# Optimization experiments

Hardware: AMD Instinct MI355X
Metric: run time of the kernel (lower is better)

## Reference

```python
import jax, jax.numpy as jnp
import numpy as np

B, S, D, H = 2, 2048, 1024, 16
HD = D // H

def setup_inputs() -> dict:
    key = jax.random.key(0)
    ks = jax.random.split(key, 9)
    s = 1.0 / np.sqrt(D)
    inp = {"x": jax.random.normal(ks[0], (B, S, D), dtype=jnp.float32)}
    for i, name in enumerate(["q", "k", "v", "o"]):
        inp[f"W_{name}"] = jax.random.uniform(ks[1 + 2 * i], (D, D), dtype=jnp.float32, minval=-s, maxval=s)
        inp[f"b_{name}"] = jax.random.uniform(ks[2 + 2 * i], (D,), dtype=jnp.float32, minval=-s, maxval=s)
    return inp


def reference(x, W_q, b_q, W_k, b_k, W_v, b_v, W_o, b_o):
    # x: [B, S, D]
    def split_heads(t):
        return t.reshape(B, S, H, HD).transpose(0, 2, 1, 3)  # [B, H, S, HD]

    Q = split_heads(x @ W_q + b_q)
    K = split_heads(x @ W_k + b_k)
    V = split_heads(x @ W_v + b_v)

    scale = 1.0 / np.sqrt(HD).astype(np.float32)
    scores = jnp.einsum("bhqd,bhkd->bhqk", Q, K) * scale  # [B, H, S, S]
    weights = jax.nn.softmax(scores, axis=-1)
    attn = jnp.einsum("bhqk,bhkd->bhqd", weights, V)  # [B, H, S, HD]
    attn = attn.transpose(0, 2, 1, 3).reshape(B, S, D)
    return attn @ W_o + b_o
```

## Files before the change

### kernel.cpp

```cpp
#include <hip/hip_runtime.h>
#include <hip/hip_bf16.h>

#define BB 2
#define SS 2048
#define DD 1024
#define HH 16
#define HD 64

typedef __attribute__((ext_vector_type(8))) short bf16x8;
typedef __attribute__((ext_vector_type(4))) float f32x4;

__device__ __forceinline__ unsigned short f2bf(float f) {
  unsigned int u = __float_as_uint(f);
  return (unsigned short)((u + 0x7FFFu + ((u >> 16) & 1u)) >> 16);
}

__device__ __forceinline__ float fast_exp2(float x) {
#if __has_builtin(__builtin_amdgcn_exp2f)
  return __builtin_amdgcn_exp2f(x);
#else
  return __expf(x * 0.6931471805599453f);
#endif
}

__device__ __forceinline__ void async_copy16(const unsigned short* gp, unsigned short* lp) {
  __builtin_amdgcn_global_load_lds(
      (const __attribute__((address_space(1))) unsigned int*)gp,
      (__attribute__((address_space(3))) unsigned int*)lp, 16, 0, 0);
}

__device__ __forceinline__ void pl32_swap(unsigned& a, unsigned& b) {
#if __has_builtin(__builtin_amdgcn_permlane32_swap)
  auto r = __builtin_amdgcn_permlane32_swap(a, b, false, false);
  a = r[0];
  b = r[1];
#else
  asm volatile("v_permlane32_swap_b32 %0, %1" : "+v"(a), "+v"(b));
#endif
}
__device__ __forceinline__ void pl16_swap(unsigned& a, unsigned& b) {
#if __has_builtin(__builtin_amdgcn_permlane16_swap)
  auto r = __builtin_amdgcn_permlane16_swap(a, b, false, false);
  a = r[0];
  b = r[1];
#else
  asm volatile("v_permlane16_swap_b32 %0, %1" : "+v"(a), "+v"(b));
#endif
}

__global__ __launch_bounds__(256) void prep_kernel(
    const float* __restrict__ x, unsigned short* __restrict__ xb,
    const float* __restrict__ W0, unsigned short* __restrict__ T0,
    const float* __restrict__ W1, unsigned short* __restrict__ T1,
    const float* __restrict__ W2, unsigned short* __restrict__ T2,
    const float* __restrict__ W3, unsigned short* __restrict__ T3) {
  const int blk = blockIdx.x;
  const int t = threadIdx.x;
  if (blk < 4096) {
    int i = blk * 1024 + t * 4;
    float4 v = *(const float4*)(x + i);
    ushort4 u;
    u.x = f2bf(v.x); u.y = f2bf(v.y); u.z = f2bf(v.z); u.w = f2bf(v.w);
    *(ushort4*)(xb + i) = u;
    return;
  }
  const int j = blk - 4096;
  const int jw = j >> 10;
  const int tb = j & 1023;
  const float* W = jw == 0 ? W0 : (jw == 1 ? W1 : (jw == 2 ? W2 : W3));
  unsigned short* T = jw == 0 ? T0 : (jw == 1 ? T1 : (jw == 2 ? T2 : T3));
  __shared__ float tile[32][33];
  int k0 = (tb & 31) * 32, n0 = (tb >> 5) * 32;
  int c = t & 31, r0 = t >> 5;
#pragma unroll
  for (int i = 0; i < 4; ++i) {
    int r = r0 + i * 8;
    tile[r][c] = W[(size_t)(k0 + r) * DD + n0 + c];
  }
  __syncthreads();
#pragma unroll
  for (int i = 0; i < 4; ++i) {
    int r = r0 + i * 8;
    T[(size_t)(n0 + r) * DD + k0 + c] = f2bf(tile[c][r]);
  }
}

template <int STORE>
__device__ __forceinline__ void gemm_core(
    const unsigned short* __restrict__ A, const unsigned short* __restrict__ BT,
    const float* __restrict__ bias, void* __restrict__ outp, float scale,
    int bm, int bn) {
  const int t = threadIdx.x;
  const int w = t >> 6;
  const int l = t & 63;
  const int wm = (w >> 1) * 64;
  const int wn = (w & 1) * 64;

  __shared__ __align__(16) unsigned short As[128 * 32];
  __shared__ __align__(16) unsigned short Bs[128 * 32];

  f32x4 acc[4][4];
#pragma unroll
  for (int i = 0; i < 4; ++i)
#pragma unroll
    for (int j = 0; j < 4; ++j) acc[i][j] = (f32x4)0.f;

  const int fr = l & 15;
  const int kg = (l >> 4) * 8;

  for (int k0 = 0; k0 < DD; k0 += 32) {
    __syncthreads();
#pragma unroll
    for (int c = 0; c < 2; ++c) {
      int e = (w * 2 + c) * 512 + l * 8;
      int row = e >> 5, kk = e & 31;
      async_copy16(A + (size_t)(bm + row) * DD + k0 + kk, As + (w * 2 + c) * 512);
      async_copy16(BT + (size_t)(bn + row) * DD + k0 + kk, Bs + (w * 2 + c) * 512);
    }
    __syncthreads();

    bf16x8 af[4], bfr[4];
#pragma unroll
    for (int i = 0; i < 4; ++i)
      af[i] = *(const bf16x8*)(As + (wm + i * 16 + fr) * 32 + kg);
#pragma unroll
    for (int j = 0; j < 4; ++j)
      bfr[j] = *(const bf16x8*)(Bs + (wn + j * 16 + fr) * 32 + kg);
#pragma unroll
    for (int i = 0; i < 4; ++i)
#pragma unroll
      for (int j = 0; j < 4; ++j)
        acc[i][j] = __builtin_amdgcn_mfma_f32_16x16x32_bf16(af[i], bfr[j], acc[i][j], 0, 0, 0);
  }

  const int col_l = l & 15;
  const int row_l = (l >> 4) * 4;

#pragma unroll
  for (int i = 0; i < 4; ++i) {
    int m_base = bm + wm + i * 16 + row_l;
#pragma unroll
    for (int j = 0; j < 4; ++j) {
      int n = bn + wn + j * 16 + col_l;
      float bv = bias[n];
      float* out = (float*)outp;
#pragma unroll
      for (int r = 0; r < 4; ++r)
        out[(size_t)(m_base + r) * DD + n] = acc[i][j][r] + bv;
    }
  }
}

__global__ __launch_bounds__(256) void out_gemm_mfma(
    const unsigned short* __restrict__ A, const unsigned short* __restrict__ WoT,
    const float* __restrict__ bo, float* __restrict__ out) {
  const int i = blockIdx.x;
  const int xcd = i & 7;
  const int slot = i >> 3;
  const int bm = (xcd + 8 * (slot >> 3)) * 128;
  const int bn = (slot & 7) * 128;
  gemm_core<0>(A, WoT, bo, (void*)out, 1.0f, bm, bn);
}

#define QPHASE(DB, KH, MH, S, VM) do {                                        \
    bf16x8 af[4];                                                             \
    _Pragma("unroll")                                                         \
    for (int ii = 0; ii < 4; ++ii) {                                          \
      int row = wm * 128 + (MH) * 64 + ii * 16 + fr;                          \
      int kb = kg16 ^ ((row & 8) ? 32 : 0) ^ ((row & 4) ? 16 : 0);            \
      af[ii] = *(const bf16x8*)((const char*)&lds[0][DB][KH][0] + row * 64 + kb); \
    }                                                                         \
    if ((MH) == 0) {                                                          \
      _Pragma("unroll")                                                       \
      for (int j = 0; j < 4; ++j) {                                           \
        int row = wn * 64 + j * 16 + fr;                                      \
        int kb = kg16 ^ ((row & 8) ? 32 : 0) ^ ((row & 4) ? 16 : 0);          \
        bfr[j] = *(const bf16x8*)((const char*)&lds[1][DB][KH][0] + row * 64 + kb); \
      }                                                                       \
    }                                                                         \
    stage_half(S);                                                            \
    asm volatile("s_barrier" ::: "memory");                                   \
    __builtin_amdgcn_s_setprio(1);                                            \
    _Pragma("unroll")                                                         \
    for (int ii = 0; ii < 4; ++ii)                                            \
      _Pragma("unroll")                                                       \
      for (int j = 0; j < 4; ++j)                                             \
        acc[(MH) * 4 + ii][j] = __builtin_amdgcn_mfma_f32_16x16x32_bf16(      \
            af[ii], bfr[j], acc[(MH) * 4 + ii][j], 0, 0, 0);                  \
    __builtin_amdgcn_s_setprio(0);                                            \
    if ((VM) == 1) asm volatile("s_waitcnt vmcnt(4)" ::: "memory");           \
    if ((VM) == 2) asm volatile("s_waitcnt vmcnt(0)" ::: "memory");           \
    asm volatile("s_barrier" ::: "memory");                                   \
  } while (0)

__global__ __launch_bounds__(512, 2) void qkv_gemm_8ph(
    const unsigned short* __restrict__ A,
    const unsigned short* __restrict__ WqT, const unsigned short* __restrict__ WkT,
    const unsigned short* __restrict__ WvT,
    const float* __restrict__ bq, const float* __restrict__ bk,
    const float* __restrict__ bv,
    unsigned short* __restrict__ Qo, unsigned short* __restrict__ Ko,
    unsigned short* __restrict__ VTo) {
  const int i = blockIdx.x;
  const int xcd = i & 7;
  const int slot = i >> 3;
  const int bmi = xcd * 2 + (slot / 12);
  const int c = slot % 12;
  const int which = c >> 2;
  const int bm = bmi * 256;
  const int bn = (c & 3) * 256;
  const unsigned short* BT = which == 0 ? WqT : (which == 1 ? WkT : WvT);
  const float* bias = which == 0 ? bq : (which == 1 ? bk : bv);

  const int t = threadIdx.x;
  const int w = t >> 6;
  const int l = t & 63;
  const int wm = w >> 2;
  const int wn = w & 3;
  const int fr = l & 15;
  const int kg16 = (l >> 4) * 16;

  __shared__ __align__(16) unsigned short lds[2][2][2][8192];

  f32x4 acc[8][4];
#pragma unroll
  for (int mi = 0; mi < 8; ++mi)
#pragma unroll
    for (int j = 0; j < 4; ++j) acc[mi][j] = (f32x4)0.f;

  auto stage_half = [&](int s) {
    if (s >= 64) return;
    const int Ts = s >> 2;
    const int db = Ts & 1;
    const int typ = s & 3;
    const int kh = typ >> 1;
    const int isB = typ & 1;
    const unsigned short* src = isB ? BT : A;
    const int rbase = isB ? bn : bm;
    unsigned short* dstbase = &lds[isB][db][kh][0];
    const int k0 = Ts * 64 + kh * 32;
#pragma unroll
    for (int j = 0; j < 2; ++j) {
      int cc = (w * 2 + j) * 64 + l;
      int row = cc >> 2;
      int ke = ((cc & 3) * 8) ^ ((row & 8) ? 16 : 0) ^ ((row & 4) ? 8 : 0);
      async_copy16(src + (size_t)(rbase + row) * DD + k0 + ke,
                   dstbase + (w * 2 + j) * 512);
    }
  };

  bf16x8 bfr[4];

  for (int s = 0; s < 6; ++s) stage_half(s);
  asm volatile("s_waitcnt vmcnt(4)" ::: "memory");
  asm volatile("s_barrier" ::: "memory");

  for (int T = 0; T < 14; ++T) {
    const int db = T & 1;
    const int sb = 4 * T + 6;
    QPHASE(db, 0, 0, sb + 0, 0);
    QPHASE(db, 0, 1, sb + 1, 0);
    QPHASE(db, 1, 0, sb + 2, 0);
    QPHASE(db, 1, 1, sb + 3, 1);
  }
  QPHASE(0, 0, 0, 62, 0);
  QPHASE(0, 0, 1, 63, 0);
  QPHASE(0, 1, 0, 64, 0);
  QPHASE(0, 1, 1, 64, 2);
  QPHASE(1, 0, 0, 64, 0);
  QPHASE(1, 0, 1, 64, 0);
  QPHASE(1, 1, 0, 64, 0);
  QPHASE(1, 1, 1, 64, 0);

  const int col_l = l & 15;
  const int row_l = (l >> 4) * 4;
  const int b_ = bm >> 11;

  if (which != 2) {
    const float scl = which == 0 ? 0.18033688011112042f : 1.0f;
    unsigned short* out = which == 0 ? Qo : Ko;
#pragma unroll
    for (int mi = 0; mi < 8; ++mi) {
      int m_base = bm + wm * 128 + mi * 16 + row_l;
#pragma unroll
      for (int j = 0; j < 4; ++j) {
        int n = bn + wn * 64 + j * 16 + col_l;
        float bv = bias[n];
        int h_ = n >> 6, hd_ = n & 63;
#pragma unroll
        for (int r = 0; r < 4; ++r) {
          int m = m_base + r;
          int b2 = m >> 11, s_ = m & 2047;
          out[(((size_t)(b2 * HH + h_) * SS) + s_) * HD + hd_] =
              f2bf((acc[mi][j][r] + bv) * scl);
        }
      }
    }
  } else {
    unsigned int* Tt = (unsigned int*)&lds[0][0][0][0];
#pragma unroll
    for (int mi = 0; mi < 8; ++mi) {
      int m2a = wm * 64 + mi * 8 + (l >> 4) * 2;
#pragma unroll
      for (int j = 0; j < 4; ++j) {
        int n = wn * 64 + j * 16 + col_l;
        float bv = bias[bn + n];
        uint2 dd;
        dd.x = (unsigned)f2bf(acc[mi][j][0] + bv) |
               ((unsigned)f2bf(acc[mi][j][1] + bv) << 16);
        dd.y = (unsigned)f2bf(acc[mi][j][2] + bv) |
               ((unsigned)f2bf(acc[mi][j][3] + bv) << 16);
        *(uint2*)(Tt + n * 128 + (m2a ^ ((n & 7) << 2))) = dd;
      }
    }
    __syncthreads();
    const int srow0 = bm & 2047;
    const int n_r = t >> 1;
    const int half = t & 1;
    const int n_glob = bn + n_r;
    const int h_ = n_glob >> 6, hd_ = n_glob & 63;
    unsigned short* ob =
        VTo + ((size_t)((b_ * HH + h_) * HD + hd_)) * SS + srow0 + half * 128;
#pragma unroll
    for (int cp = 0; cp < 16; ++cp) {
      uint4 v = *(const uint4*)(Tt + n_r * 128 +
                                ((half * 64 + cp * 4) ^ ((n_r & 7) << 2)));
      *(uint4*)(ob + cp * 8) = v;
    }
  }
}

__global__ __launch_bounds__(512, 4) void flash_attn_mfma(
    const unsigned short* __restrict__ Q,
    const unsigned short* __restrict__ K,
    const unsigned short* __restrict__ VT,
    unsigned short* __restrict__ ctx) {
  const int bh = blockIdx.x;
  const int qt = blockIdx.y;
  const int b  = bh >> 4;
  const int h  = bh & 15;
  const int t  = threadIdx.x;
  const int w  = t >> 6;
  const int l  = t & 63;
  const int wg = w & 3;
  const int wh = w >> 2;
  const int g  = l >> 4;
  const int ln = l & 15;

  const unsigned short* Qp = Q + ((size_t)bh * SS + (size_t)qt * 128 + wg * 32) * HD;
  const unsigned short* Kp = K + (size_t)bh * SS * HD;
  const unsigned short* Vp = VT + (size_t)bh * HD * SS;

  __shared__ __align__(16) unsigned short Ks[2][2][64 * 64];
  __shared__ __align__(16) unsigned short Vs[2][2][64 * 64];

  bf16x8 qf[2][2];
#pragma unroll
  for (int nt = 0; nt < 2; ++nt)
#pragma unroll
    for (int kb = 0; kb < 2; ++kb)
      qf[nt][kb] = *(const bf16x8*)(Qp + (nt * 16 + ln) * HD + kb * 32 + g * 8);

  f32x4 o[2][4];
#pragma unroll
  for (int nt = 0; nt < 2; ++nt)
#pragma unroll
    for (int mt = 0; mt < 4; ++mt) o[nt][mt] = (f32x4)0.f;
  float rs[2] = {0.f, 0.f};

  auto stage2 = [&](int kt2, int db) {
    const int cidx = t;
    const int row = cidx >> 3, cc = cidx & 7;
    const int gcc = cc ^ (row & 7);
    const int k0 = kt2 * 128;
    async_copy16(Kp + (size_t)(k0 + row) * HD + gcc * 8, &Ks[0][db][w * 512]);
    async_copy16(Kp + (size_t)(k0 + 64 + row) * HD + gcc * 8, &Ks[1][db][w * 512]);
    async_copy16(Vp + (size_t)row * SS + k0 + gcc * 8, &Vs[0][db][w * 512]);
    async_copy16(Vp + (size_t)row * SS + k0 + 64 + gcc * 8, &Vs[1][db][w * 512]);
  };

  stage2(0, 0);
  for (int kt2 = 0; kt2 < SS / 128; ++kt2) {
    const int db = kt2 & 1;
    __syncthreads();
    if (kt2 + 1 < SS / 128) stage2(kt2 + 1, db ^ 1);

    const unsigned short* Kst = &Ks[wh][db][0];
    const unsigned short* Vst = &Vs[wh][db][0];

    f32x4 st[2][4];
#pragma unroll
    for (int nt = 0; nt < 2; ++nt)
#pragma unroll
      for (int mt = 0; mt < 4; ++mt) st[nt][mt] = (f32x4)0.f;
#pragma unroll
    for (int kb = 0; kb < 2; ++kb)
#pragma unroll
      for (int mt = 0; mt < 4; ++mt) {
        int row = mt * 16 + ln;
        bf16x8 ka = *(const bf16x8*)(&Kst[row * 64 + (((kb * 4 + g) ^ (row & 7)) * 8)]);
        st[0][mt] = __builtin_amdgcn_mfma_f32_16x16x32_bf16(ka, qf[0][kb], st[0][mt], 0, 0, 0);
        st[1][mt] = __builtin_amdgcn_mfma_f32_16x16x32_bf16(ka, qf[1][kb], st[1][mt], 0, 0, 0);
      }

    unsigned Sd[2][4][2];
#pragma unroll
    for (int nt = 0; nt < 2; ++nt) {
#pragma unroll
      for (int mt = 0; mt < 4; ++mt) {
        float p0 = fast_exp2(st[nt][mt][0]);
        float p1 = fast_exp2(st[nt][mt][1]);
        float p2 = fast_exp2(st[nt][mt][2]);
        float p3 = fast_exp2(st[nt][mt][3]);
        Sd[nt][mt][0] = __builtin_amdgcn_perm(__float_as_uint(p1), __float_as_uint(p0),
                                              0x07060302u);
        Sd[nt][mt][1] = __builtin_amdgcn_perm(__float_as_uint(p3), __float_as_uint(p2),
                                              0x07060302u);
        rs[nt] += (p0 + p1) + (p2 + p3);
      }
#pragma unroll
      for (int m1 = 0; m1 < 2; ++m1)
#pragma unroll
        for (int p = 0; p < 2; ++p)
          pl32_swap(Sd[nt][2 * m1][p], Sd[nt][2 * m1 + 1][p]);
#pragma unroll
      for (int m1 = 0; m1 < 2; ++m1)
#pragma unroll
        for (int p = 0; p < 2; ++p)
          pl16_swap(Sd[nt][2 * m1][p], Sd[nt][2 * m1 + 1][p]);
    }

#pragma unroll
    for (int kb = 0; kb < 2; ++kb) {
      bf16x8 pbv[2];
#pragma unroll
      for (int nt = 0; nt < 2; ++nt) {
        union { unsigned u[4]; bf16x8 v; } cu;
        cu.u[0] = Sd[nt][2 * kb][0];
        cu.u[1] = Sd[nt][2 * kb][1];
        cu.u[2] = Sd[nt][2 * kb + 1][0];
        cu.u[3] = Sd[nt][2 * kb + 1][1];
        pbv[nt] = cu.v;
      }
#pragma unroll
      for (int mt = 0; mt < 4; ++mt) {
        int row = mt * 16 + ln;
        bf16x8 va = *(const bf16x8*)(&Vst[row * 64 + (((kb * 4 + g) ^ (row & 7)) * 8)]);
        o[0][mt] = __builtin_amdgcn_mfma_f32_16x16x32_bf16(va, pbv[0], o[0][mt], 0, 0, 0);
        o[1][mt] = __builtin_amdgcn_mfma_f32_16x16x32_bf16(va, pbv[1], o[1][mt], 0, 0, 0);
      }
    }
  }

  __syncthreads();
  {
    float* ored = (float*)&Vs[0][0][0];
    float* rred = (float*)&Ks[0][0][0];
    float* rb = ored + (wg * 64 + l) * 32;
    float* sb = rred + (wg * 64 + l) * 2;
    if (wh == 1) {
#pragma unroll
      for (int nt = 0; nt < 2; ++nt)
#pragma unroll
        for (int mt = 0; mt < 4; ++mt) {
          int idx = nt * 4 + mt;
          *(f32x4*)(rb + ((unsigned)(idx ^ (l & 7)) * 4)) = o[nt][mt];
        }
      sb[0] = rs[0];
      sb[1] = rs[1];
    }
    __syncthreads();
    if (wh == 1) return;
#pragma unroll
    for (int nt = 0; nt < 2; ++nt)
#pragma unroll
      for (int mt = 0; mt < 4; ++mt) {
        int idx = nt * 4 + mt;
        f32x4 pv = *(const f32x4*)(rb + ((unsigned)(idx ^ (l & 7)) * 4));
        o[nt][mt] += pv;
      }
    rs[0] += sb[0];
    rs[1] += sb[1];
  }

#pragma unroll
  for (int nt = 0; nt < 2; ++nt) {
    float lsum = rs[nt];
    lsum += __shfl_xor(lsum, 16, 64);
    lsum += __shfl_xor(lsum, 32, 64);
    float inv = 1.f / lsum;
    int srow = qt * 128 + wg * 32 + nt * 16 + ln;
    unsigned short* cb = ctx + (size_t)(b * SS + srow) * DD + h * HD;
#pragma unroll
    for (int mt = 0; mt < 4; ++mt) {
      ushort4 u4;
      u4.x = f2bf(o[nt][mt][0] * inv);
      u4.y = f2bf(o[nt][mt][1] * inv);
      u4.z = f2bf(o[nt][mt][2] * inv);
      u4.w = f2bf(o[nt][mt][3] * inv);
      *(ushort4*)(cb + mt * 16 + 4 * g) = u4;
    }
  }
}

extern "C" void kernel_launch(void* const* d_in, const int* in_sizes, int n_in,
                              void* d_out, int out_size, void* d_ws, size_t ws_size,
                              hipStream_t stream) {
  const float* x  = (const float*)d_in[0];
  const float* Wq = (const float*)d_in[1];
  const float* bq = (const float*)d_in[2];
  const float* Wk = (const float*)d_in[3];
  const float* bk = (const float*)d_in[4];
  const float* Wv = (const float*)d_in[5];
  const float* bv = (const float*)d_in[6];
  const float* Wo = (const float*)d_in[7];
  const float* bo = (const float*)d_in[8];
  float* out = (float*)d_out;

  const size_t ELEMS = (size_t)BB * SS * DD;
  char* ws = (char*)d_ws;
  unsigned short* xb   = (unsigned short*)ws;  ws += ELEMS * 2;
  unsigned short* WqT  = (unsigned short*)ws;  ws += (size_t)DD * DD * 2;
  unsigned short* WkT  = (unsigned short*)ws;  ws += (size_t)DD * DD * 2;
  unsigned short* WvT  = (unsigned short*)ws;  ws += (size_t)DD * DD * 2;
  unsigned short* WoT  = (unsigned short*)ws;  ws += (size_t)DD * DD * 2;
  unsigned short* Qb   = (unsigned short*)ws;  ws += ELEMS * 2;
  unsigned short* Kb   = (unsigned short*)ws;  ws += ELEMS * 2;
  unsigned short* VbT  = (unsigned short*)ws;  ws += ELEMS * 2;
  unsigned short* ctxb = (unsigned short*)ws;  ws += ELEMS * 2;

  prep_kernel<<<8192, 256, 0, stream>>>(x, xb, Wq, WqT, Wk, WkT, Wv, WvT, Wo, WoT);

  qkv_gemm_8ph<<<192, 512, 0, stream>>>(xb, WqT, WkT, WvT, bq, bk, bv,
                                        Qb, Kb, VbT);

  dim3 attn_grid(BB * HH, SS / 128);
  flash_attn_mfma<<<attn_grid, 512, 0, stream>>>(Qb, Kb, VbT, ctxb);

  out_gemm_mfma<<<256, 256, 0, stream>>>(ctxb, WoT, bo, out);
}
```

Measured before the change: 194.2 us.

## Halve flash-attention KV tile per iteration to cut LDS and registers

The flash attention kernel now stages 64 keys per iteration instead of 128. Each wave half handles 32 keys, which halves the score and probability register arrays and the K/V shared-memory buffers. A new V layout with a 32-column swizzle comes with it. Launch bounds are raised to 8 blocks per CU to exploit the lower LDS and register use. In exchange there are twice as many barrier-synchronised iterations with less MFMA work each, and occupancy may be capped by registers.

```diff
diff --git a/kernel.cpp b/kernel.cpp
--- a/kernel.cpp
+++ b/kernel.cpp
@@ -330,7 +330,7 @@
   }
 }
 
-__global__ __launch_bounds__(512, 4) void flash_attn_mfma(
+__global__ __launch_bounds__(512, 8) void flash_attn_mfma(
     const unsigned short* __restrict__ Q,
     const unsigned short* __restrict__ K,
     const unsigned short* __restrict__ VT,
@@ -351,8 +351,8 @@
   const unsigned short* Kp = K + (size_t)bh * SS * HD;
   const unsigned short* Vp = VT + (size_t)bh * HD * SS;
 
-  __shared__ __align__(16) unsigned short Ks[2][2][64 * 64];
-  __shared__ __align__(16) unsigned short Vs[2][2][64 * 64];
+  __shared__ __align__(16) unsigned short smem[2][2][2][2048];
+  __shared__ __align__(16) float rred[4 * 64 * 2];
 
   bf16x8 qf[2][2];
 #pragma unroll
@@ -368,46 +368,54 @@
     for (int mt = 0; mt < 4; ++mt) o[nt][mt] = (f32x4)0.f;
   float rs[2] = {0.f, 0.f};
 
-  auto stage2 = [&](int kt2, int db) {
-    const int cidx = t;
-    const int row = cidx >> 3, cc = cidx & 7;
-    const int gcc = cc ^ (row & 7);
-    const int k0 = kt2 * 128;
-    async_copy16(Kp + (size_t)(k0 + row) * HD + gcc * 8, &Ks[0][db][w * 512]);
-    async_copy16(Kp + (size_t)(k0 + 64 + row) * HD + gcc * 8, &Ks[1][db][w * 512]);
-    async_copy16(Vp + (size_t)row * SS + k0 + gcc * 8, &Vs[0][db][w * 512]);
-    async_copy16(Vp + (size_t)row * SS + k0 + 64 + gcc * 8, &Vs[1][db][w * 512]);
+  const int sp  = w >> 2;
+  const int sq  = w & 3;
+  auto stage = [&](int kt, int db) {
+    {
+      const int idx = sq * 64 + l;
+      const int row = idx >> 3, cc = idx & 7;
+      const int gcc = cc ^ (row & 7);
+      async_copy16(Kp + (size_t)(kt * 64 + sp * 32 + row) * HD + gcc * 8,
+                   &smem[0][sp][db][sq * 512]);
+    }
+    {
+      const int idx = sq * 64 + l;
+      const int row = idx >> 2, c2 = idx & 3;
+      const int gc2 = c2 ^ ((row >> 1) & 3);
+      async_copy16(Vp + (size_t)row * SS + kt * 64 + sp * 32 + gc2 * 8,
+                   &smem[1][sp][db][sq * 512]);
+    }
   };
 
-  stage2(0, 0);
-  for (int kt2 = 0; kt2 < SS / 128; ++kt2) {
-    const int db = kt2 & 1;
+  stage(0, 0);
+  for (int kt = 0; kt < SS / 64; ++kt) {
+    const int db = kt & 1;
     __syncthreads();
-    if (kt2 + 1 < SS / 128) stage2(kt2 + 1, db ^ 1);
-
-    const unsigned short* Kst = &Ks[wh][db][0];
-    const unsigned short* Vst = &Vs[wh][db][0];
-
-    f32x4 st[2][4];
+    if (kt + 1 < SS / 64) stage(kt + 1, db ^ 1);
+
+    const unsigned short* Kst = &smem[0][wh][db][0];
+    const unsigned short* Vst = &smem[1][wh][db][0];
+
+    f32x4 st[2][2];
 #pragma unroll
     for (int nt = 0; nt < 2; ++nt)
 #pragma unroll
-      for (int mt = 0; mt < 4; ++mt) st[nt][mt] = (f32x4)0.f;
+      for (int mt = 0; mt < 2; ++mt) st[nt][mt] = (f32x4)0.f;
 #pragma unroll
     for (int kb = 0; kb < 2; ++kb)
 #pragma unroll
-      for (int mt = 0; mt < 4; ++mt) {
+      for (int mt = 0; mt < 2; ++mt) {
         int row = mt * 16 + ln;
         bf16x8 ka = *(const bf16x8*)(&Kst[row * 64 + (((kb * 4 + g) ^ (row & 7)) * 8)]);
         st[0][mt] = __builtin_amdgcn_mfma_f32_16x16x32_bf16(ka, qf[0][kb], st[0][mt], 0, 0, 0);
         st[1][mt] = __builtin_amdgcn_mfma_f32_16x16x32_bf16(ka, qf[1][kb], st[1][mt], 0, 0, 0);
       }
 
-    unsigned Sd[2][4][2];
+    unsigned Sd[2][2][2];
 #pragma unroll
     for (int nt = 0; nt < 2; ++nt) {
 #pragma unroll
-      for (int mt = 0; mt < 4; ++mt) {
+      for (int mt = 0; mt < 2; ++mt) {
         float p0 = fast_exp2(st[nt][mt][0]);
         float p1 = fast_exp2(st[nt][mt][1]);
         float p2 = fast_exp2(st[nt][mt][2]);
@@ -419,43 +427,33 @@
         rs[nt] += (p0 + p1) + (p2 + p3);
       }
 #pragma unroll
-      for (int m1 = 0; m1 < 2; ++m1)
-#pragma unroll
-        for (int p = 0; p < 2; ++p)
-          pl32_swap(Sd[nt][2 * m1][p], Sd[nt][2 * m1 + 1][p]);
-#pragma unroll
-      for (int m1 = 0; m1 < 2; ++m1)
-#pragma unroll
-        for (int p = 0; p < 2; ++p)
-          pl16_swap(Sd[nt][2 * m1][p], Sd[nt][2 * m1 + 1][p]);
-    }
-
-#pragma unroll
-    for (int kb = 0; kb < 2; ++kb) {
-      bf16x8 pbv[2];
-#pragma unroll
-      for (int nt = 0; nt < 2; ++nt) {
-        union { unsigned u[4]; bf16x8 v; } cu;
-        cu.u[0] = Sd[nt][2 * kb][0];
-        cu.u[1] = Sd[nt][2 * kb][1];
-        cu.u[2] = Sd[nt][2 * kb + 1][0];
-        cu.u[3] = Sd[nt][2 * kb + 1][1];
-        pbv[nt] = cu.v;
-      }
-#pragma unroll
-      for (int mt = 0; mt < 4; ++mt) {
-        int row = mt * 16 + ln;
-        bf16x8 va = *(const bf16x8*)(&Vst[row * 64 + (((kb * 4 + g) ^ (row & 7)) * 8)]);
-        o[0][mt] = __builtin_amdgcn_mfma_f32_16x16x32_bf16(va, pbv[0], o[0][mt], 0, 0, 0);
-        o[1][mt] = __builtin_amdgcn_mfma_f32_16x16x32_bf16(va, pbv[1], o[1][mt], 0, 0, 0);
-      }
+      for (int p = 0; p < 2; ++p) pl32_swap(Sd[nt][0][p], Sd[nt][1][p]);
+#pragma unroll
+      for (int p = 0; p < 2; ++p) pl16_swap(Sd[nt][0][p], Sd[nt][1][p]);
+    }
+
+    bf16x8 pbv[2];
+#pragma unroll
+    for (int nt = 0; nt < 2; ++nt) {
+      union { unsigned u[4]; bf16x8 v; } cu;
+      cu.u[0] = Sd[nt][0][0];
+      cu.u[1] = Sd[nt][0][1];
+      cu.u[2] = Sd[nt][1][0];
+      cu.u[3] = Sd[nt][1][1];
+      pbv[nt] = cu.v;
+    }
+#pragma unroll
+    for (int mt = 0; mt < 4; ++mt) {
+      int row = mt * 16 + ln;
+      bf16x8 va = *(const bf16x8*)(&Vst[row * 32 + ((g ^ ((row >> 1) & 3)) * 8)]);
+      o[0][mt] = __builtin_amdgcn_mfma_f32_16x16x32_bf16(va, pbv[0], o[0][mt], 0, 0, 0);
+      o[1][mt] = __builtin_amdgcn_mfma_f32_16x16x32_bf16(va, pbv[1], o[1][mt], 0, 0, 0);
     }
   }
 
   __syncthreads();
   {
-    float* ored = (float*)&Vs[0][0][0];
-    float* rred = (float*)&Ks[0][0][0];
+    float* ored = (float*)&smem[0][0][0][0];
     float* rb = ored + (wg * 64 + l) * 32;
     float* sb = rred + (wg * 64 + l) * 2;
     if (wh == 1) {
```

After: 310.9 us. 60.1% more time.
